# Kernel tuning notes

Hardware: AMD Instinct MI355X
Metric: run time of the kernel (lower is better)

## Reference

```python
import jax, jax.numpy as jnp
import numpy as np

N_NODES = 100000
N_EDGES = 1600000
DIM = 64          # num_features == hidden_dim
N_LAYERS = 5
N_GRAPHS = 1024
EMB = DIM * N_LAYERS  # 320
BN_EPS = 1e-5


def setup_inputs() -> dict:
    key = jax.random.key(0)
    ks = jax.random.split(key, 16)
    s = 0.05
    return {
        "x": jax.random.normal(ks[0], (N_NODES, DIM), dtype=jnp.float32),
        "edge_index": jax.random.randint(ks[1], (2, N_EDGES), 0, N_NODES, dtype=jnp.int32),
        "edge_weight": jax.random.uniform(ks[2], (N_EDGES,), dtype=jnp.float32),
        "batch": jnp.sort(jax.random.randint(ks[3], (N_NODES,), 0, N_GRAPHS, dtype=jnp.int32)),
        # stacked per-layer GIN MLP params: nn = Linear(d,d) -> ReLU -> Linear(d,d)
        "W1s": jax.random.normal(ks[4], (N_LAYERS, DIM, DIM), dtype=jnp.float32) * s,
        "b1s": jnp.zeros((N_LAYERS, DIM), dtype=jnp.float32),
        "W2s": jax.random.normal(ks[5], (N_LAYERS, DIM, DIM), dtype=jnp.float32) * s,
        "b2s": jnp.zeros((N_LAYERS, DIM), dtype=jnp.float32),
        # BatchNorm1d affine params (init: weight=1, bias=0)
        "gammas": jnp.ones((N_LAYERS, DIM), dtype=jnp.float32),
        "betas": jnp.zeros((N_LAYERS, DIM), dtype=jnp.float32),
        # projection head: Linear(EMB,EMB) -> ReLU -> Linear(EMB,EMB)
        "pW1": jax.random.normal(ks[6], (EMB, EMB), dtype=jnp.float32) * s,
        "pb1": jnp.zeros((EMB,), dtype=jnp.float32),
        "pW2": jax.random.normal(ks[7], (EMB, EMB), dtype=jnp.float32) * s,
        "pb2": jnp.zeros((EMB,), dtype=jnp.float32),
    }


def _encoder(x, src, dst, edge_weight, batch,
             W1s, b1s, W2s, b2s, gammas, betas):
    h = x
    pooled = []
    for i in range(N_LAYERS):
        # WGINConv (eps=0): h_out = nn(h + sum_{j->i} w_ij * h_j)
        msg = jax.ops.segment_sum(h[src] * edge_weight[:, None], dst,
                                  num_segments=N_NODES)  # [N, D]
        z = h + msg
        z = jnp.maximum(z @ W1s[i] + b1s[i], 0.0) @ W2s[i] + b2s[i]
        h = jnp.maximum(z, 0.0)  # F.relu after conv
        # BatchNorm1d (training mode: batch stats over nodes, biased var)
        mean = jnp.mean(h, axis=0)
        var = jnp.var(h, axis=0)
        h = (h - mean) * jax.lax.rsqrt(var + BN_EPS) * gammas[i] + betas[i]
        pooled.append(h)
    # global_mean_pool per layer, then concat along feature dim
    counts = jax.ops.segment_sum(jnp.ones((N_NODES,), h.dtype), batch,
                                 num_segments=N_GRAPHS)
    counts = jnp.maximum(counts, 1.0)[:, None]
    xpool = [jax.ops.segment_sum(h, batch, num_segments=N_GRAPHS) / counts
             for h in pooled]
    return jnp.concatenate(xpool, axis=1)  # [G, L*D]


def reference(x, edge_index, edge_weight, batch,
              W1s, b1s, W2s, b2s, gammas, betas,
              pW1, pb1, pW2, pb2):
    src, dst = edge_index[0], edge_index[1]
    y = _encoder(x, src, dst, edge_weight, batch,
                 W1s, b1s, W2s, b2s, gammas, betas)
    # proj_head: Linear -> ReLU -> Linear
    y = jnp.maximum(y @ pW1 + pb1, 0.0) @ pW2 + pb2
    return y
```

## Files before the change

### kernel.cpp

```cpp
#include <hip/hip_runtime.h>

#define NN 100000
#define NE 1600000
#define D 64
#define NL 5
#define NG 1024
#define EMBD 320
#define BN_EPS 1e-5f
#define SCAN_NB ((NN + 255) / 256)
#define GIN_NB ((NN + 63) / 64)
#define SRCB 7
#define M2 (NN * SRCB)
#define SCAN2_NB ((M2 + 255) / 256)

__device__ __forceinline__ unsigned short bf16rne(float f) {
  unsigned u = __float_as_uint(f);
  unsigned r = u + 0x7FFFu + ((u >> 16) & 1u);
  return (unsigned short)(r >> 16);
}
__device__ __forceinline__ float bflo(int v) {
  return __uint_as_float(((unsigned)v) << 16);
}
__device__ __forceinline__ float bfhi(int v) {
  return __uint_as_float(((unsigned)v) & 0xFFFF0000u);
}

__global__ __launch_bounds__(256) void k_cvt(const float* __restrict__ in,
                                             unsigned short* __restrict__ outb) {
  int i = blockIdx.x * 256 + threadIdx.x;
  if (i >= NN * 16) return;
  float4 v = ((const float4*)in)[i];
  ushort4 o;
  o.x = bf16rne(v.x); o.y = bf16rne(v.y); o.z = bf16rne(v.z); o.w = bf16rne(v.w);
  ((ushort4*)outb)[i] = o;
}

__global__ __launch_bounds__(256) void k_gbound(const int* __restrict__ batch,
                                                int* __restrict__ gstart) {
  int i = blockIdx.x * 256 + threadIdx.x;
  if (i >= NN) return;
  int b = batch[i];
  int bp = (i == 0) ? -1 : batch[i - 1];
  for (int g = bp + 1; g <= b; ++g) gstart[g] = i;
  if (i == NN - 1) {
    for (int g = b + 1; g <= NG; ++g) gstart[g] = NN;
  }
}

__global__ __launch_bounds__(256) void k_hist(const int* __restrict__ src,
                                              const int* __restrict__ dst,
                                              int* __restrict__ deg) {
  int e = blockIdx.x * 256 + threadIdx.x;
  if (e >= NE) return;
  int s = __builtin_nontemporal_load(src + e);
  int d = __builtin_nontemporal_load(dst + e);
  atomicAdd(&deg[d * SRCB + (s >> 14)], 1);
}

__global__ __launch_bounds__(256) void k_scan1(const int* __restrict__ deg,
                                               int* __restrict__ bsums) {
  __shared__ int sh[256];
  int i = blockIdx.x * 256 + threadIdx.x;
  sh[threadIdx.x] = (i < M2) ? deg[i] : 0;
  __syncthreads();
  for (int off = 128; off > 0; off >>= 1) {
    if (threadIdx.x < off) sh[threadIdx.x] += sh[threadIdx.x + off];
    __syncthreads();
  }
  if (threadIdx.x == 0) bsums[blockIdx.x] = sh[0];
}

__global__ __launch_bounds__(1024) void k_scan2(int* __restrict__ bsums) {
  __shared__ int sh[1024];
  int t = threadIdx.x;
  int loc[3];
  int s = 0;
#pragma unroll
  for (int i = 0; i < 3; ++i) {
    int idx = t * 3 + i;
    loc[i] = s;
    if (idx < SCAN2_NB) s += bsums[idx];
  }
  sh[t] = s;
  __syncthreads();
  for (int off = 1; off < 1024; off <<= 1) {
    int u = (t >= off) ? sh[t - off] : 0;
    __syncthreads();
    sh[t] += u;
    __syncthreads();
  }
  int base = sh[t] - s;
#pragma unroll
  for (int i = 0; i < 3; ++i) {
    int idx = t * 3 + i;
    if (idx < SCAN2_NB) bsums[idx] = base + loc[i];
  }
}

__global__ __launch_bounds__(256) void k_scan3(int* __restrict__ row_ptr,
                                               int* __restrict__ cursor,
                                               const int* __restrict__ bsums) {
  __shared__ int sh[256];
  int t = threadIdx.x;
  int i = blockIdx.x * 256 + t;
  int v = (i < M2) ? row_ptr[i] : 0;
  sh[t] = v;
  __syncthreads();
  for (int off = 1; off < 256; off <<= 1) {
    int u = (t >= off) ? sh[t - off] : 0;
    __syncthreads();
    sh[t] += u;
    __syncthreads();
  }
  int excl = sh[t] - v + bsums[blockIdx.x];
  if (i < M2) {
    row_ptr[i] = excl;
    cursor[i] = excl;
    if (i == M2 - 1) row_ptr[M2] = excl + v;
  }
}

__global__ __launch_bounds__(256) void k_fill(const int* __restrict__ src,
                                              const int* __restrict__ dst,
                                              const float* __restrict__ w,
                                              int* __restrict__ cursor,
                                              long long* __restrict__ epair) {
  int e = blockIdx.x * 256 + threadIdx.x;
  if (e >= NE) return;
  int s = __builtin_nontemporal_load(src + e);
  int d = __builtin_nontemporal_load(dst + e);
  float we = __builtin_nontemporal_load(w + e);
  int slot = atomicAdd(&cursor[d * SRCB + (s >> 14)], 1);
  long long p = (long long)(unsigned)s |
                ((long long)(unsigned)__float_as_int(we) << 32);
  epair[slot] = p;
}

#define ACC8(CA, CB, WE)                                                      \
  a0.x = fmaf(bflo(CA.x), WE, a0.x); a0.y = fmaf(bfhi(CA.x), WE, a0.y);       \
  a0.z = fmaf(bflo(CA.y), WE, a0.z); a0.w = fmaf(bfhi(CA.y), WE, a0.w);       \
  a1.x = fmaf(bflo(CA.z), WE, a1.x); a1.y = fmaf(bfhi(CA.z), WE, a1.y);       \
  a1.z = fmaf(bflo(CA.w), WE, a1.z); a1.w = fmaf(bfhi(CA.w), WE, a1.w);       \
  a2.x = fmaf(bflo(CB.x), WE, a2.x); a2.y = fmaf(bfhi(CB.x), WE, a2.y);       \
  a2.z = fmaf(bflo(CB.y), WE, a2.z); a2.w = fmaf(bfhi(CB.y), WE, a2.w);       \
  a3.x = fmaf(bflo(CB.z), WE, a3.x); a3.y = fmaf(bfhi(CB.z), WE, a3.y);       \
  a3.z = fmaf(bflo(CB.w), WE, a3.z); a3.w = fmaf(bfhi(CB.w), WE, a3.w);

__global__ __launch_bounds__(256, 6) void k_gin(const float* __restrict__ x0,
                                                const unsigned short* __restrict__ hbf,
                                                unsigned short* __restrict__ gbf,
                                                const int* __restrict__ row_ptr,
                                                const long long* __restrict__ epair,
                                                const int* __restrict__ batch_,
                                                const int* __restrict__ gstart_,
                                                float* __restrict__ pooledraw,
                                                int layer,
                                                const float* __restrict__ W1,
                                                const float* __restrict__ b1,
                                                const float* __restrict__ W2,
                                                const float* __restrict__ b2,
                                                const float* __restrict__ statsP,
                                                const float* __restrict__ gammaP,
                                                const float* __restrict__ betaP,
                                                int first,
                                                float* __restrict__ statsL) {
  __shared__ float zin[64 * 65];
  __shared__ float sW[32 * 64];
  __shared__ float sb[64];
  __shared__ float wsumS[64];
  __shared__ float scA[64], sbA[64];
  __shared__ float psum[256];
  const int t = threadIdx.x;
  const int nb = blockIdx.x * 64;
  const int nr = t >> 4, fc = t & 15;

  for (int i = t; i < 2048; i += 256) sW[i] = W1[i];
  if (t < 64) {
    sb[t] = b1[t];
    if (!first) {
      float m = statsP[t] * (1.f / NN);
      float v = fmaxf(statsP[64 + t] * (1.f / NN) - m * m, 0.f);
      float sc = gammaP[t] * rsqrtf(v + BN_EPS);
      scA[t] = sc;
      sbA[t] = betaP[t] - m * sc;
    }
  }

  {
    const int nl = t >> 2;
    const int q = t & 3;
    const int n = nb + nl;
    float4 a0 = {0.f, 0.f, 0.f, 0.f}, a1 = a0, a2 = a0, a3 = a0;
    float wsum = 0.f;
    if (n < NN) {
      const int beg = row_ptr[n * SRCB], end = row_ptr[n * SRCB + SRCB];
      int i = beg;
      for (; i + 2 <= end; i += 2) {
        long long e0 = __builtin_nontemporal_load(epair + i);
        long long e1 = __builtin_nontemporal_load(epair + i + 1);
        int s0 = (int)(e0 & 0xFFFFFFFFll);
        float w0 = __int_as_float((int)(e0 >> 32));
        int s1 = (int)(e1 & 0xFFFFFFFFll);
        float w1 = __int_as_float((int)(e1 >> 32));
        const int4* p0 = (const int4*)(hbf + (size_t)s0 * D);
        const int4* p1 = (const int4*)(hbf + (size_t)s1 * D);
        int4 r0a = p0[2 * q], r0b = p0[2 * q + 1];
        int4 r1a = p1[2 * q], r1b = p1[2 * q + 1];
        ACC8(r0a, r0b, w0)
        wsum += w0;
        ACC8(r1a, r1b, w1)
        wsum += w1;
      }
      for (; i < end; ++i) {
        long long e0 = __builtin_nontemporal_load(epair + i);
        int s0 = (int)(e0 & 0xFFFFFFFFll);
        float w0 = __int_as_float((int)(e0 >> 32));
        const int4* p0 = (const int4*)(hbf + (size_t)s0 * D);
        int4 r0a = p0[2 * q], r0b = p0[2 * q + 1];
        ACC8(r0a, r0b, w0)
        wsum += w0;
      }
      if (first) {
        const float4* own = (const float4*)(x0 + (size_t)n * D) + q * 4;
        float4 o0 = own[0], o1 = own[1], o2 = own[2], o3 = own[3];
        a0.x += o0.x; a0.y += o0.y; a0.z += o0.z; a0.w += o0.w;
        a1.x += o1.x; a1.y += o1.y; a1.z += o1.z; a1.w += o1.w;
        a2.x += o2.x; a2.y += o2.y; a2.z += o2.z; a2.w += o2.w;
        a3.x += o3.x; a3.y += o3.y; a3.z += o3.z; a3.w += o3.w;
      } else {
        const int4* hp = (const int4*)(hbf + (size_t)n * D);
        int4 c0 = hp[2 * q], c1 = hp[2 * q + 1];
        a0.x += bflo(c0.x); a0.y += bfhi(c0.x);
        a0.z += bflo(c0.y); a0.w += bfhi(c0.y);
        a1.x += bflo(c0.z); a1.y += bfhi(c0.z);
        a1.z += bflo(c0.w); a1.w += bfhi(c0.w);
        a2.x += bflo(c1.x); a2.y += bfhi(c1.x);
        a2.z += bflo(c1.y); a2.w += bfhi(c1.y);
        a3.x += bflo(c1.z); a3.y += bfhi(c1.z);
        a3.z += bflo(c1.w); a3.w += bfhi(c1.w);
      }
    }
    float* zr = &zin[nl * 65 + q * 16];
    *(float4*)(zr + 0) = a0;
    *(float4*)(zr + 4) = a1;
    *(float4*)(zr + 8) = a2;
    *(float4*)(zr + 12) = a3;
    if (q == 0) wsumS[nl] = wsum;
  }
  __syncthreads();

  if (!first) {
#pragma unroll
    for (int pass = 0; pass < 4; ++pass) {
      int idx = pass * 1024 + t * 4;
      int r = idx >> 6, c = idx & 63;
      float wp1 = 1.f + wsumS[r];
      float4 z = *(float4*)&zin[r * 65 + c];
      z.x = fmaf(z.x, scA[c + 0], sbA[c + 0] * wp1);
      z.y = fmaf(z.y, scA[c + 1], sbA[c + 1] * wp1);
      z.z = fmaf(z.z, scA[c + 2], sbA[c + 2] * wp1);
      z.w = fmaf(z.w, scA[c + 3], sbA[c + 3] * wp1);
      *(float4*)&zin[r * 65 + c] = z;
    }
    __syncthreads();
  }

#define GEMM_HALF(ACC, KBASE)                                                 \
  _Pragma("unroll 2") for (int kc = 0; kc < 8; ++kc) {                        \
    float4 zv[4], wv[4];                                                      \
    _Pragma("unroll") for (int i = 0; i < 4; ++i)                             \
        zv[i] = *(float4*)&zin[(nr * 4 + i) * 65 + ((KBASE) + kc) * 4];       \
    _Pragma("unroll") for (int kk = 0; kk < 4; ++kk)                          \
        wv[kk] = *(float4*)&sW[(kc * 4 + kk) * 64 + fc * 4];                  \
    _Pragma("unroll") for (int i = 0; i < 4; ++i) {                           \
      ACC[i].x = fmaf(zv[i].x, wv[0].x, ACC[i].x);                            \
      ACC[i].y = fmaf(zv[i].x, wv[0].y, ACC[i].y);                            \
      ACC[i].z = fmaf(zv[i].x, wv[0].z, ACC[i].z);                            \
      ACC[i].w = fmaf(zv[i].x, wv[0].w, ACC[i].w);                            \
      ACC[i].x = fmaf(zv[i].y, wv[1].x, ACC[i].x);                            \
      ACC[i].y = fmaf(zv[i].y, wv[1].y, ACC[i].y);                            \
      ACC[i].z = fmaf(zv[i].y, wv[1].z, ACC[i].z);                            \
      ACC[i].w = fmaf(zv[i].y, wv[1].w, ACC[i].w);                            \
      ACC[i].x = fmaf(zv[i].z, wv[2].x, ACC[i].x);                            \
      ACC[i].y = fmaf(zv[i].z, wv[2].y, ACC[i].y);                            \
      ACC[i].z = fmaf(zv[i].z, wv[2].z, ACC[i].z);                            \
      ACC[i].w = fmaf(zv[i].z, wv[2].w, ACC[i].w);                            \
      ACC[i].x = fmaf(zv[i].w, wv[3].x, ACC[i].x);                            \
      ACC[i].y = fmaf(zv[i].w, wv[3].y, ACC[i].y);                            \
      ACC[i].z = fmaf(zv[i].w, wv[3].z, ACC[i].z);                            \
      ACC[i].w = fmaf(zv[i].w, wv[3].w, ACC[i].w);                            \
    }                                                                         \
  }

#define RELU4(ACC)                                                            \
  _Pragma("unroll") for (int i = 0; i < 4; ++i) {                             \
    ACC[i].x = fmaxf(ACC[i].x, 0.f);                                          \
    ACC[i].y = fmaxf(ACC[i].y, 0.f);                                          \
    ACC[i].z = fmaxf(ACC[i].z, 0.f);                                          \
    ACC[i].w = fmaxf(ACC[i].w, 0.f);                                          \
  }

  float4 acc[4];
  {
    float4 bias = *(float4*)&sb[fc * 4];
#pragma unroll
    for (int i = 0; i < 4; ++i) acc[i] = bias;
  }
  GEMM_HALF(acc, 0)
  __syncthreads();
  for (int i = t; i < 2048; i += 256) sW[i] = W1[2048 + i];
  __syncthreads();
  GEMM_HALF(acc, 8)
  RELU4(acc)
  __syncthreads();

#pragma unroll
  for (int i = 0; i < 4; ++i) *(float4*)&zin[(nr * 4 + i) * 65 + fc * 4] = acc[i];
  for (int i = t; i < 2048; i += 256) sW[i] = W2[i];
  if (t < 64) sb[t] = b2[t];
  __syncthreads();

  float4 acc2[4];
  {
    float4 bias = *(float4*)&sb[fc * 4];
#pragma unroll
    for (int i = 0; i < 4; ++i) acc2[i] = bias;
  }
  GEMM_HALF(acc2, 0)
  __syncthreads();
  for (int i = t; i < 2048; i += 256) sW[i] = W2[2048 + i];
  __syncthreads();
  GEMM_HALF(acc2, 8)
  RELU4(acc2)
  __syncthreads();

  float4 s4 = {0.f, 0.f, 0.f, 0.f}, q4 = {0.f, 0.f, 0.f, 0.f};
#pragma unroll
  for (int i = 0; i < 4; ++i) {
    int n = nb + nr * 4 + i;
    *(float4*)&zin[(nr * 4 + i) * 65 + fc * 4] = acc2[i];
    if (n < NN) {
      ushort4 ob;
      ob.x = bf16rne(acc2[i].x);
      ob.y = bf16rne(acc2[i].y);
      ob.z = bf16rne(acc2[i].z);
      ob.w = bf16rne(acc2[i].w);
      *(ushort4*)(gbf + (size_t)n * D + fc * 4) = ob;
      s4.x += acc2[i].x; s4.y += acc2[i].y; s4.z += acc2[i].z; s4.w += acc2[i].w;
      q4.x = fmaf(acc2[i].x, acc2[i].x, q4.x);
      q4.y = fmaf(acc2[i].y, acc2[i].y, q4.y);
      q4.z = fmaf(acc2[i].z, acc2[i].z, q4.z);
      q4.w = fmaf(acc2[i].w, acc2[i].w, q4.w);
    }
  }
  __syncthreads();

  {
    const int nbend = (nb + 64 < NN) ? nb + 64 : NN;
    const int gs = batch_[nb];
    const int ge = batch_[nbend - 1];
    const int c = t & 63, qr = t >> 6;
    for (int g = gs; g <= ge; ++g) {
      int a = gstart_[g];
      int b = gstart_[g + 1];
      a = (a > nb) ? a - nb : 0;
      b = (b < nbend) ? b - nb : nbend - nb;
      float p = 0.f;
      for (int r = a + qr; r < b; r += 4) p += zin[r * 65 + c];
      psum[t] = p;
      __syncthreads();
      if (t < 64) {
        float tot = psum[t] + psum[t + 64] + psum[t + 128] + psum[t + 192];
        unsafeAtomicAdd(&pooledraw[(size_t)g * EMBD + layer * D + t], tot);
      }
      __syncthreads();
    }
  }

#pragma unroll
  for (int m = 16; m <= 32; m <<= 1) {
    s4.x += __shfl_xor(s4.x, m, 64); s4.y += __shfl_xor(s4.y, m, 64);
    s4.z += __shfl_xor(s4.z, m, 64); s4.w += __shfl_xor(s4.w, m, 64);
    q4.x += __shfl_xor(q4.x, m, 64); q4.y += __shfl_xor(q4.y, m, 64);
    q4.z += __shfl_xor(q4.z, m, 64); q4.w += __shfl_xor(q4.w, m, 64);
  }
  int wv_ = t >> 6;
  if ((t & 63) < 16) {
    *(float4*)&zin[wv_ * 64 + fc * 4] = s4;
    *(float4*)&zin[256 + wv_ * 64 + fc * 4] = q4;
  }
  __syncthreads();
  if (t < 64) {
    float S = zin[t] + zin[64 + t] + zin[128 + t] + zin[192 + t];
    float Q = zin[256 + t] + zin[320 + t] + zin[384 + t] + zin[448 + t];
    unsafeAtomicAdd(&statsL[t], S);
    unsafeAtomicAdd(&statsL[64 + t], Q);
  }
#undef GEMM_HALF
#undef RELU4
}

__global__ __launch_bounds__(EMBD) void k_proj(const float* __restrict__ pooledraw,
                                               const int* __restrict__ gstart,
                                               const float* __restrict__ stats,
                                               const float* __restrict__ gammas,
                                               const float* __restrict__ betas,
                                               const float* __restrict__ pW1,
                                               const float* __restrict__ pb1,
                                               const float* __restrict__ pW2,
                                               const float* __restrict__ pb2,
                                               float* __restrict__ out) {
  __shared__ float row[EMBD];
  __shared__ float y1[EMBD];
  int g = blockIdx.x, j = threadIdx.x;
  {
    int L = j >> 6, f = j & 63;
    float m = stats[L * 128 + f] * (1.f / NN);
    float v = fmaxf(stats[L * 128 + 64 + f] * (1.f / NN) - m * m, 0.f);
    float sc = gammas[L * D + f] * rsqrtf(v + BN_EPS);
    float sb = betas[L * D + f] - m * sc;
    int cnt = gstart[g + 1] - gstart[g];
    float inv = 1.0f / (float)(cnt > 1 ? cnt : 1);
    row[j] = fmaf(pooledraw[(size_t)g * EMBD + j] * inv, sc, sb);
  }
  __syncthreads();
  float acc = pb1[j];
#pragma unroll 4
  for (int k = 0; k < EMBD; ++k) acc = fmaf(row[k], pW1[(size_t)k * EMBD + j], acc);
  y1[j] = fmaxf(acc, 0.f);
  __syncthreads();
  acc = pb2[j];
#pragma unroll 4
  for (int k = 0; k < EMBD; ++k) acc = fmaf(y1[k], pW2[(size_t)k * EMBD + j], acc);
  out[(size_t)g * EMBD + j] = acc;
}

extern "C" void kernel_launch(void* const* d_in, const int* in_sizes, int n_in,
                              void* d_out, int out_size, void* d_ws, size_t ws_size,
                              hipStream_t stream) {
  const float* x = (const float*)d_in[0];
  const int* ei = (const int*)d_in[1];
  const float* ew = (const float*)d_in[2];
  const int* batch = (const int*)d_in[3];
  const float* W1s = (const float*)d_in[4];
  const float* b1s = (const float*)d_in[5];
  const float* W2s = (const float*)d_in[6];
  const float* b2s = (const float*)d_in[7];
  const float* gammas = (const float*)d_in[8];
  const float* betas = (const float*)d_in[9];
  const float* pW1 = (const float*)d_in[10];
  const float* pb1 = (const float*)d_in[11];
  const float* pW2 = (const float*)d_in[12];
  const float* pb2 = (const float*)d_in[13];
  const int* srcv = ei;
  const int* dstv = ei + NE;

  char* ws = (char*)d_ws;
  float* stats = (float*)ws;
  float* pooledraw = stats + NL * 128;
  int* gstart = (int*)(pooledraw + (size_t)NG * EMBD);
  int* row_ptr = gstart + NG + 1;
  int* cursor = row_ptr + M2 + 1;
  long long* epair = (long long*)(cursor + M2);
  int* bsums = (int*)(epair + NE);
  unsigned short* hbfA = (unsigned short*)(bsums + SCAN2_NB);
  unsigned short* hbfB = hbfA + (size_t)NN * D;

  hipMemsetAsync(row_ptr, 0, (M2 + 1) * sizeof(int), stream);
  hipMemsetAsync(stats, 0,
                 (NL * 128 + (size_t)NG * EMBD) * sizeof(float), stream);
  k_hist<<<(NE + 255) / 256, 256, 0, stream>>>(srcv, dstv, row_ptr);
  k_scan1<<<SCAN2_NB, 256, 0, stream>>>(row_ptr, bsums);
  k_scan2<<<1, 1024, 0, stream>>>(bsums);
  k_scan3<<<SCAN2_NB, 256, 0, stream>>>(row_ptr, cursor, bsums);
  k_fill<<<(NE + 255) / 256, 256, 0, stream>>>(srcv, dstv, ew, cursor, epair);
  k_gbound<<<SCAN_NB, 256, 0, stream>>>(batch, gstart);
  k_cvt<<<(NN * 16 + 255) / 256, 256, 0, stream>>>(x, hbfA);

  unsigned short* bfin = hbfA;
  unsigned short* bfout = hbfB;
  for (int L = 0; L < NL; ++L) {
    k_gin<<<GIN_NB, 256, 0, stream>>>(x, bfin, bfout, row_ptr, epair,
                                      batch, gstart, pooledraw, L,
                                      W1s + L * D * D, b1s + L * D,
                                      W2s + L * D * D, b2s + L * D,
                                      stats + (L > 0 ? (L - 1) * 128 : 0),
                                      gammas + (L > 0 ? (L - 1) * D : 0),
                                      betas + (L > 0 ? (L - 1) * D : 0),
                                      L == 0 ? 1 : 0,
                                      stats + L * 128);
    unsigned short* tmpb = bfin;
    bfin = bfout;
    bfout = tmpb;
  }
  k_proj<<<NG, EMBD, 0, stream>>>(pooledraw, gstart, stats, gammas, betas,
                                  pW1, pb1, pW2, pb2, (float*)d_out);
}
```

Before: 797.9 us.

## Replace global-atomic CSR build with two-level LDS-based bucket sort

Replaces the per-edge global atomic histogram and fill over a 700K-entry key table with a two-pass counting sort. Edges are first bucketed by destination block of 512 nodes, using per-chunk LDS histograms and a scanned chunk-by-bucket table. Each bucket is then sorted locally in shared memory by (node, source-range) key to produce row_ptr and epair. This avoids heavy contended global atomics and the large memset, at the cost of an extra temporary edge buffer and extra kernel passes. Within-key edge order becomes nondeterministic, as it already was.

```diff
diff --git a/kernel.cpp b/kernel.cpp
--- a/kernel.cpp
+++ b/kernel.cpp
@@ -11,7 +11,12 @@
 #define GIN_NB ((NN + 63) / 64)
 #define SRCB 7
 #define M2 (NN * SRCB)
-#define SCAN2_NB ((M2 + 255) / 256)
+#define CH 4096
+#define NCH ((NE + CH - 1) / CH)
+#define NBK 196
+#define TBL (NBK * NCH)
+#define SCANT_NB ((TBL + 255) / 256)
+#define NKEY 3584
 
 __device__ __forceinline__ unsigned short bf16rne(float f) {
   unsigned u = __float_as_uint(f);
@@ -47,21 +52,25 @@
   }
 }
 
-__global__ __launch_bounds__(256) void k_hist(const int* __restrict__ src,
-                                              const int* __restrict__ dst,
-                                              int* __restrict__ deg) {
-  int e = blockIdx.x * 256 + threadIdx.x;
-  if (e >= NE) return;
-  int s = __builtin_nontemporal_load(src + e);
-  int d = __builtin_nontemporal_load(dst + e);
-  atomicAdd(&deg[d * SRCB + (s >> 14)], 1);
-}
-
-__global__ __launch_bounds__(256) void k_scan1(const int* __restrict__ deg,
-                                               int* __restrict__ bsums) {
+__global__ __launch_bounds__(256) void k_passA(const int* __restrict__ dst,
+                                               int* __restrict__ table) {
+  __shared__ int lh[NBK];
+  for (int i = threadIdx.x; i < NBK; i += 256) lh[i] = 0;
+  __syncthreads();
+  int base = blockIdx.x * CH;
+  int lim = base + CH < NE ? base + CH : NE;
+  for (int i = base + threadIdx.x; i < lim; i += 256)
+    atomicAdd(&lh[__builtin_nontemporal_load(dst + i) >> 9], 1);
+  __syncthreads();
+  for (int i = threadIdx.x; i < NBK; i += 256)
+    table[i * NCH + blockIdx.x] = lh[i];
+}
+
+__global__ __launch_bounds__(256) void k_scanT1(const int* __restrict__ tab,
+                                                int* __restrict__ bsums) {
   __shared__ int sh[256];
   int i = blockIdx.x * 256 + threadIdx.x;
-  sh[threadIdx.x] = (i < M2) ? deg[i] : 0;
+  sh[threadIdx.x] = (i < TBL) ? tab[i] : 0;
   __syncthreads();
   for (int off = 128; off > 0; off >>= 1) {
     if (threadIdx.x < off) sh[threadIdx.x] += sh[threadIdx.x + off];
@@ -70,40 +79,27 @@
   if (threadIdx.x == 0) bsums[blockIdx.x] = sh[0];
 }
 
-__global__ __launch_bounds__(1024) void k_scan2(int* __restrict__ bsums) {
-  __shared__ int sh[1024];
+__global__ __launch_bounds__(512) void k_scanT2(int* __restrict__ bsums) {
+  __shared__ int sh[512];
   int t = threadIdx.x;
-  int loc[3];
-  int s = 0;
-#pragma unroll
-  for (int i = 0; i < 3; ++i) {
-    int idx = t * 3 + i;
-    loc[i] = s;
-    if (idx < SCAN2_NB) s += bsums[idx];
-  }
-  sh[t] = s;
-  __syncthreads();
-  for (int off = 1; off < 1024; off <<= 1) {
+  int v = (t < SCANT_NB) ? bsums[t] : 0;
+  sh[t] = v;
+  __syncthreads();
+  for (int off = 1; off < 512; off <<= 1) {
     int u = (t >= off) ? sh[t - off] : 0;
     __syncthreads();
     sh[t] += u;
     __syncthreads();
   }
-  int base = sh[t] - s;
-#pragma unroll
-  for (int i = 0; i < 3; ++i) {
-    int idx = t * 3 + i;
-    if (idx < SCAN2_NB) bsums[idx] = base + loc[i];
-  }
-}
-
-__global__ __launch_bounds__(256) void k_scan3(int* __restrict__ row_ptr,
-                                               int* __restrict__ cursor,
-                                               const int* __restrict__ bsums) {
+  if (t < SCANT_NB) bsums[t] = sh[t] - v;
+}
+
+__global__ __launch_bounds__(256) void k_scanT3(int* __restrict__ tab,
+                                                const int* __restrict__ bsums) {
   __shared__ int sh[256];
   int t = threadIdx.x;
   int i = blockIdx.x * 256 + t;
-  int v = (i < M2) ? row_ptr[i] : 0;
+  int v = (i < TBL) ? tab[i] : 0;
   sh[t] = v;
   __syncthreads();
   for (int off = 1; off < 256; off <<= 1) {
@@ -112,28 +108,90 @@
     sh[t] += u;
     __syncthreads();
   }
-  int excl = sh[t] - v + bsums[blockIdx.x];
-  if (i < M2) {
-    row_ptr[i] = excl;
-    cursor[i] = excl;
-    if (i == M2 - 1) row_ptr[M2] = excl + v;
-  }
-}
-
-__global__ __launch_bounds__(256) void k_fill(const int* __restrict__ src,
-                                              const int* __restrict__ dst,
-                                              const float* __restrict__ w,
-                                              int* __restrict__ cursor,
-                                              long long* __restrict__ epair) {
-  int e = blockIdx.x * 256 + threadIdx.x;
-  if (e >= NE) return;
-  int s = __builtin_nontemporal_load(src + e);
-  int d = __builtin_nontemporal_load(dst + e);
-  float we = __builtin_nontemporal_load(w + e);
-  int slot = atomicAdd(&cursor[d * SRCB + (s >> 14)], 1);
-  long long p = (long long)(unsigned)s |
-                ((long long)(unsigned)__float_as_int(we) << 32);
-  epair[slot] = p;
+  if (i < TBL) tab[i] = sh[t] - v + bsums[blockIdx.x];
+}
+
+__global__ __launch_bounds__(256) void k_passB(const int* __restrict__ src,
+                                               const int* __restrict__ dst,
+                                               const float* __restrict__ w,
+                                               const int* __restrict__ table,
+                                               long long* __restrict__ tmp) {
+  __shared__ int lbase[NBK];
+  __shared__ int lcur[NBK];
+  for (int i = threadIdx.x; i < NBK; i += 256) {
+    lbase[i] = table[i * NCH + blockIdx.x];
+    lcur[i] = 0;
+  }
+  __syncthreads();
+  int base = blockIdx.x * CH;
+  int lim = base + CH < NE ? base + CH : NE;
+  for (int i = base + threadIdx.x; i < lim; i += 256) {
+    int s = __builtin_nontemporal_load(src + i);
+    int d = __builtin_nontemporal_load(dst + i);
+    float we = __builtin_nontemporal_load(w + i);
+    int b = d >> 9;
+    int slot = lbase[b] + atomicAdd(&lcur[b], 1);
+    long long p = (long long)(unsigned)(s | ((d & 511) << 17)) |
+                  ((long long)(unsigned)__float_as_int(we) << 32);
+    tmp[slot] = p;
+  }
+}
+
+__global__ __launch_bounds__(512) void k_passC(const long long* __restrict__ tmp,
+                                               const int* __restrict__ table,
+                                               int* __restrict__ row_ptr,
+                                               long long* __restrict__ epair) {
+  __shared__ int kh[NKEY];
+  __shared__ int aux[512];
+  const int t = threadIdx.x;
+  const int b = blockIdx.x;
+  const int bb = table[b * NCH];
+  const int be = (b == NBK - 1) ? NE : table[(b + 1) * NCH];
+  for (int i = t; i < NKEY; i += 512) kh[i] = 0;
+  __syncthreads();
+  for (int i = bb + t; i < be; i += 512) {
+    long long e = tmp[i];
+    int lo = (int)e;
+    int ln = (lo >> 17) & 511;
+    int s = lo & 0x1FFFF;
+    atomicAdd(&kh[ln * 7 + (s >> 14)], 1);
+  }
+  __syncthreads();
+  int loc[7];
+  int ssum = 0;
+#pragma unroll
+  for (int j = 0; j < 7; ++j) {
+    loc[j] = ssum;
+    ssum += kh[t * 7 + j];
+  }
+  aux[t] = ssum;
+  __syncthreads();
+  for (int off = 1; off < 512; off <<= 1) {
+    int u = (t >= off) ? aux[t - off] : 0;
+    __syncthreads();
+    aux[t] += u;
+    __syncthreads();
+  }
+  int excl = aux[t] - ssum;
+#pragma unroll
+  for (int j = 0; j < 7; ++j) kh[t * 7 + j] = excl + loc[j];
+  __syncthreads();
+  const int nodebase = b * 512;
+  for (int i = t; i < NKEY; i += 512) {
+    int node = nodebase + i / 7;
+    if (node < NN) row_ptr[(size_t)node * 7 + (i % 7)] = bb + kh[i];
+  }
+  if (b == NBK - 1 && t == 0) row_ptr[M2] = NE;
+  __syncthreads();
+  for (int i = bb + t; i < be; i += 512) {
+    long long e = tmp[i];
+    int lo = (int)e;
+    int ln = (lo >> 17) & 511;
+    int s = lo & 0x1FFFF;
+    int slot = bb + atomicAdd(&kh[ln * 7 + (s >> 14)], 1);
+    epair[slot] = (long long)(unsigned)s |
+                  (e & 0xFFFFFFFF00000000ll);
+  }
 }
 
 #define ACC8(CA, CB, WE)                                                      \
@@ -460,20 +518,21 @@
   float* pooledraw = stats + NL * 128;
   int* gstart = (int*)(pooledraw + (size_t)NG * EMBD);
   int* row_ptr = gstart + NG + 1;
-  int* cursor = row_ptr + M2 + 1;
-  long long* epair = (long long*)(cursor + M2);
-  int* bsums = (int*)(epair + NE);
-  unsigned short* hbfA = (unsigned short*)(bsums + SCAN2_NB);
+  int* table = row_ptr + M2 + 1;
+  int* bsums = table + TBL;
+  long long* tmp = (long long*)(bsums + SCANT_NB + 1);
+  long long* epair = tmp + NE;
+  unsigned short* hbfA = (unsigned short*)(epair + NE);
   unsigned short* hbfB = hbfA + (size_t)NN * D;
 
-  hipMemsetAsync(row_ptr, 0, (M2 + 1) * sizeof(int), stream);
   hipMemsetAsync(stats, 0,
                  (NL * 128 + (size_t)NG * EMBD) * sizeof(float), stream);
-  k_hist<<<(NE + 255) / 256, 256, 0, stream>>>(srcv, dstv, row_ptr);
-  k_scan1<<<SCAN2_NB, 256, 0, stream>>>(row_ptr, bsums);
-  k_scan2<<<1, 1024, 0, stream>>>(bsums);
-  k_scan3<<<SCAN2_NB, 256, 0, stream>>>(row_ptr, cursor, bsums);
-  k_fill<<<(NE + 255) / 256, 256, 0, stream>>>(srcv, dstv, ew, cursor, epair);
+  k_passA<<<NCH, 256, 0, stream>>>(dstv, table);
+  k_scanT1<<<SCANT_NB, 256, 0, stream>>>(table, bsums);
+  k_scanT2<<<1, 512, 0, stream>>>(bsums);
+  k_scanT3<<<SCANT_NB, 256, 0, stream>>>(table, bsums);
+  k_passB<<<NCH, 256, 0, stream>>>(srcv, dstv, ew, table, tmp);
+  k_passC<<<NBK, 512, 0, stream>>>(tmp, table, row_ptr, epair);
   k_gbound<<<SCAN_NB, 256, 0, stream>>>(batch, gstart);
   k_cvt<<<(NN * 16 + 255) / 256, 256, 0, stream>>>(x, hbfA);
 
```

New measurement: 673.1 us. 15.6% less time.
